# Kernel tuning notes

Hardware: AMD Instinct MI355X
Metric: run time of the kernel (lower is better)

Reference implementation:

```python
import jax, jax.numpy as jnp
import numpy as np

B, T, U, V = 8, 128, 64, 1024
BLANK = V - 1  # blank=-1 resolves to last class index


def setup_inputs() -> dict:
    key = jax.random.key(0)
    k1, k2, k3, k4 = jax.random.split(key, 4)
    logits = jax.random.normal(k1, (B, T, U + 1, V), dtype=jnp.float32)
    targets = jax.random.randint(k2, (B, U), 0, V - 1, dtype=jnp.int32)  # exclude blank
    logit_lengths = jax.random.randint(k3, (B,), T // 2, T + 1, dtype=jnp.int32)
    target_lengths = jax.random.randint(k4, (B,), U // 2, U + 1, dtype=jnp.int32)
    return {
        "logits": logits,
        "targets": targets,
        "logit_lengths": logit_lengths,
        "target_lengths": target_lengths,
    }


def _rnnt_neglogp(logits, targets, logit_lengths, target_lengths, blank):
    """RNNT forward-variable DP (Graves 2012). Returns per-sample -log p(y|x)."""
    Bn, Tn, U1, Vn = logits.shape
    Un = U1 - 1
    lp = jax.nn.log_softmax(logits, axis=-1)  # fused_log_softmax=True
    lp_blank = lp[..., blank]                                  # (B, T, U+1)
    idx = jnp.broadcast_to(targets[:, None, :, None], (Bn, Tn, Un, 1))
    lp_emit = jnp.take_along_axis(lp[:, :, :Un, :], idx, axis=-1)[..., 0]  # (B, T, U)

    # alpha[t, u]: log-prob of emitting first u labels using first t frames.
    # alpha[0, u] = sum_{v<u} emit(0, v)
    row0 = jnp.concatenate(
        [jnp.zeros((Bn, 1), lp.dtype), jnp.cumsum(lp_emit[:, 0, :], axis=-1)], axis=1
    )  # (B, U+1)

    def inner(a_prev, x):
        # a[u] = logaddexp(alpha[t-1,u] + blank(t-1,u),  a[u-1] + emit(t,u-1))
        b_u, e_u = x
        a_new = jnp.logaddexp(b_u, a_prev + e_u)
        return a_new, a_new

    def outer(prev_row, x):
        blank_prev, emit_t = x  # (B, U+1), (B, U)
        b_term = prev_row + blank_prev  # vertical (blank) transition term
        _, rest = jax.lax.scan(
            inner, b_term[:, 0], (b_term[:, 1:].T, emit_t.T)
        )  # rest: (U, B)
        new_row = jnp.concatenate([b_term[:, :1], rest.T], axis=1)  # (B, U+1)
        return new_row, new_row

    xs = (
        jnp.swapaxes(lp_blank[:, :-1, :], 0, 1),  # (T-1, B, U+1)
        jnp.swapaxes(lp_emit[:, 1:, :], 0, 1),    # (T-1, B, U)
    )
    _, rows = jax.lax.scan(outer, row0, xs)
    alpha = jnp.concatenate([row0[None], rows], axis=0)  # (T, B, U+1)

    bidx = jnp.arange(Bn)
    t_last = logit_lengths - 1
    u_last = target_lengths
    a_end = alpha[t_last, bidx, u_last]
    final_blank = lp_blank[bidx, t_last, u_last]
    return -(a_end + final_blank)


def reference(logits, targets, logit_lengths, target_lengths):
    return _rnnt_neglogp(logits, targets, logit_lengths, target_lengths, BLANK)
```

## Files before the change

### kernel.cpp

```cpp
#include <hip/hip_runtime.h>
#include <hip/hip_bf16.h>

#define BB 8
#define TT 128
#define UU 64
#define VV 1024
#define U1 65
#define NROWS (BB * TT * U1)
#define NDIAG (TT + UU)
#define DSZ (NDIAG * U1)
#define NPROD (NROWS / 4)
#define KPF 8

typedef unsigned long long ull;

__device__ __forceinline__ float wave_sum64(float v) {
#pragma unroll
    for (int off = 32; off; off >>= 1) v += __shfl_xor(v, off, 64);
    return v;
}

__device__ __forceinline__ float2 ldP(const ull* Pb, int idx) {
    union { ull u; float2 f; } c;
    c.u = __hip_atomic_load(Pb + idx, __ATOMIC_RELAXED, __HIP_MEMORY_SCOPE_AGENT);
    return c.f;
}

__device__ __forceinline__ int diag_need(int c) {
    return min(c, 64) - max(0, c - 127) + 1;
}

__device__ __forceinline__ void wait_diag(const unsigned int* cb, int c) {
    const int nd = diag_need(c);
    int guard = 0;
    while ((int)__hip_atomic_load(cb + c, __ATOMIC_RELAXED,
                                  __HIP_MEMORY_SCOPE_AGENT) < nd) {
        __builtin_amdgcn_s_sleep(1);
        if (++guard > (1 << 22)) break;
    }
}

__global__ __launch_bounds__(256) void rnnt_fused_kernel(
    const float* __restrict__ logits, const int* __restrict__ targets,
    const int* __restrict__ logit_lengths, const int* __restrict__ target_lengths,
    ull* __restrict__ P, unsigned int* __restrict__ cnt,
    float* __restrict__ out) {

    if (blockIdx.x >= BB) {
        const int wave = threadIdx.x >> 6;
        const int lane = threadIdx.x & 63;
        const int row  = (blockIdx.x - BB) * 4 + wave;
        const int b   = row / (TT * U1);
        const int rem = row - b * (TT * U1);
        const int t   = rem / U1;
        const int u   = rem - t * U1;

        const float4* p4 = (const float4*)(logits + (size_t)row * VV);
        float4 x0 = p4[lane];
        float4 x1 = p4[lane + 64];
        float4 x2 = p4[lane + 128];
        float4 x3 = p4[lane + 192];

        float s = __expf(x0.x) + __expf(x0.y) + __expf(x0.z) + __expf(x0.w)
                + __expf(x1.x) + __expf(x1.y) + __expf(x1.z) + __expf(x1.w)
                + __expf(x2.x) + __expf(x2.y) + __expf(x2.z) + __expf(x2.w)
                + __expf(x3.x) + __expf(x3.y) + __expf(x3.z) + __expf(x3.w);
        s = wave_sum64(s);
        const float lse = __logf(s);

        const float blankv = __shfl(x3.w, 63, 64) - lse;
        float emitv = 0.f;
        if (u < UU) {
            const int tgt = targets[b * UU + u];
            const int qq = tgt >> 2, grp = qq >> 6, sl = qq & 63, c4 = tgt & 3;
            float4 g4 = (grp == 0) ? x0 : (grp == 1) ? x1 : (grp == 2) ? x2 : x3;
            float cv = (c4 == 0) ? g4.x : (c4 == 1) ? g4.y : (c4 == 2) ? g4.z : g4.w;
            emitv = __shfl(cv, sl, 64) - lse;
        }
        if (lane == 0) {
            union { ull u; float2 f; } pk;
            pk.f = make_float2(blankv, emitv);
            const int d = t + u;
            __hip_atomic_store(P + (size_t)b * DSZ + d * U1 + u, pk.u,
                               __ATOMIC_RELAXED, __HIP_MEMORY_SCOPE_AGENT);
            asm volatile("s_waitcnt vmcnt(0)" ::: "memory");
            __hip_atomic_fetch_add(cnt + b * NDIAG + d, 1u,
                                   __ATOMIC_RELAXED, __HIP_MEMORY_SCOPE_AGENT);
        }
        return;
    }

    if (threadIdx.x >= 64) return;
    const int b = blockIdx.x;
    const int l = threadIdx.x;
    const ull* Pb = P + (size_t)b * DSZ;
    const unsigned int* cb = cnt + b * NDIAG;
    const int tl = logit_lengths[b] - 1;
    const int ul = target_lengths[b];
    const int Dfin = tl + ul;

    const float NEG = -1e30f;
    float aprev   = (l == 0) ? 0.f : NEG;
    float aprev64 = NEG;
    float res = 0.f;

    float2 ring[KPF], ring64[KPF];
#pragma unroll
    for (int k = 0; k < KPF; ++k) {
        wait_diag(cb, k);
        ring[k]   = ldP(Pb, k * U1 + l);
        ring64[k] = ldP(Pb, k * U1 + 64);
    }

    for (int base = 1; base <= NDIAG - 1; base += KPF) {
#pragma unroll
        for (int s = 0; s < KPF; ++s) {
            const int d = base + s;
            if (d > NDIAG - 1) break;
            float2 pr   = ring[s];
            float2 p64v = ring64[s];
            float edl = __shfl_up(pr.y, 1, 64);
            float al  = __shfl_up(aprev, 1, 64);
            const int t = d - l;
            float va = (t >= 1) ? aprev + pr.x : NEG;
            float vb = (l >= 1) ? al + edl : NEG;
            float mm = fmaxf(va, vb);
            float r  = mm + __logf(__expf(va - mm) + __expf(vb - mm));
            r = (t >= 0 && t < TT) ? r : NEG;
            const int t64 = d - 64;
            float va64 = (t64 >= 1) ? aprev64 + p64v.x : NEG;
            float vb64 = aprev + pr.y;
            float mm64 = fmaxf(va64, vb64);
            float r64  = mm64 + __logf(__expf(va64 - mm64) + __expf(vb64 - mm64));
            r64 = (t64 >= 0) ? r64 : NEG;
            if (d == Dfin) {
                if (ul < 64) { if (l == ul) res = r; }
                else if (l == 63) res = r64;
            }
            aprev = r; aprev64 = r64;
            const int c2 = d - 1 + KPF;
            if (c2 <= NDIAG - 2) {
                wait_diag(cb, c2);
                ring[s]   = ldP(Pb, c2 * U1 + l);
                ring64[s] = ldP(Pb, c2 * U1 + 64);
            }
        }
    }

    const float rr = __shfl(res, (ul < 64) ? ul : 63, 64);
    if (l == 0) {
        wait_diag(cb, Dfin);
        out[b] = -(rr + ldP(Pb, Dfin * U1 + ul).x);
    }
}

extern "C" void kernel_launch(void* const* d_in, const int* in_sizes, int n_in,
                              void* d_out, int out_size, void* d_ws, size_t ws_size,
                              hipStream_t stream) {
    const float* logits         = (const float*)d_in[0];
    const int*   targets        = (const int*)d_in[1];
    const int*   logit_lengths  = (const int*)d_in[2];
    const int*   target_lengths = (const int*)d_in[3];
    float* outp = (float*)d_out;

    ull* P = (ull*)d_ws;
    unsigned int* cnt = (unsigned int*)((char*)d_ws + (1 << 20));

    hipMemsetAsync(cnt, 0, BB * NDIAG * sizeof(unsigned int), stream);
    rnnt_fused_kernel<<<BB + NPROD, 256, 0, stream>>>(
        logits, targets, logit_lengths, target_lengths, P, cnt, outp);
}
```

Before: 470.3 us.

## Replace per-diagonal counters with sentinel-valued data polling for producer-consumer sync

```diff
diff --git a/kernel.cpp b/kernel.cpp
--- a/kernel.cpp
+++ b/kernel.cpp
@@ -13,6 +13,7 @@
 #define KPF 8
 
 typedef unsigned long long ull;
+#define SENT32 0xFFFFFFFFu
 
 __device__ __forceinline__ float wave_sum64(float v) {
 #pragma unroll
@@ -20,31 +21,20 @@
     return v;
 }
 
-__device__ __forceinline__ float2 ldP(const ull* Pb, int idx) {
-    union { ull u; float2 f; } c;
-    c.u = __hip_atomic_load(Pb + idx, __ATOMIC_RELAXED, __HIP_MEMORY_SCOPE_AGENT);
-    return c.f;
+__device__ __forceinline__ ull ldPu(const ull* Pb, int idx) {
+    return __hip_atomic_load(Pb + idx, __ATOMIC_RELAXED, __HIP_MEMORY_SCOPE_AGENT);
 }
-
-__device__ __forceinline__ int diag_need(int c) {
-    return min(c, 64) - max(0, c - 127) + 1;
+__device__ __forceinline__ bool nrdy(ull v) {
+    return ((unsigned)(v >> 32) == SENT32) | ((unsigned)v == SENT32);
 }
-
-__device__ __forceinline__ void wait_diag(const unsigned int* cb, int c) {
-    const int nd = diag_need(c);
-    int guard = 0;
-    while ((int)__hip_atomic_load(cb + c, __ATOMIC_RELAXED,
-                                  __HIP_MEMORY_SCOPE_AGENT) < nd) {
-        __builtin_amdgcn_s_sleep(1);
-        if (++guard > (1 << 22)) break;
-    }
+__device__ __forceinline__ float2 u2f(ull v) {
+    union { ull u; float2 f; } c; c.u = v; return c.f;
 }
 
 __global__ __launch_bounds__(256) void rnnt_fused_kernel(
     const float* __restrict__ logits, const int* __restrict__ targets,
     const int* __restrict__ logit_lengths, const int* __restrict__ target_lengths,
-    ull* __restrict__ P, unsigned int* __restrict__ cnt,
-    float* __restrict__ out) {
+    ull* __restrict__ P, float* __restrict__ out) {
 
     if (blockIdx.x >= BB) {
         const int wave = threadIdx.x >> 6;
@@ -80,12 +70,8 @@
         if (lane == 0) {
             union { ull u; float2 f; } pk;
             pk.f = make_float2(blankv, emitv);
-            const int d = t + u;
-            __hip_atomic_store(P + (size_t)b * DSZ + d * U1 + u, pk.u,
+            __hip_atomic_store(P + (size_t)b * DSZ + (t + u) * U1 + u, pk.u,
                                __ATOMIC_RELAXED, __HIP_MEMORY_SCOPE_AGENT);
-            asm volatile("s_waitcnt vmcnt(0)" ::: "memory");
-            __hip_atomic_fetch_add(cnt + b * NDIAG + d, 1u,
-                                   __ATOMIC_RELAXED, __HIP_MEMORY_SCOPE_AGENT);
         }
         return;
     }
@@ -94,7 +80,6 @@
     const int b = blockIdx.x;
     const int l = threadIdx.x;
     const ull* Pb = P + (size_t)b * DSZ;
-    const unsigned int* cb = cnt + b * NDIAG;
     const int tl = logit_lengths[b] - 1;
     const int ul = target_lengths[b];
     const int Dfin = tl + ul;
@@ -104,12 +89,11 @@
     float aprev64 = NEG;
     float res = 0.f;
 
-    float2 ring[KPF], ring64[KPF];
+    ull ring[KPF], ring64[KPF];
 #pragma unroll
     for (int k = 0; k < KPF; ++k) {
-        wait_diag(cb, k);
-        ring[k]   = ldP(Pb, k * U1 + l);
-        ring64[k] = ldP(Pb, k * U1 + 64);
+        ring[k]   = ldPu(Pb, k * U1 + l);
+        ring64[k] = ldPu(Pb, k * U1 + 64);
     }
 
     for (int base = 1; base <= NDIAG - 1; base += KPF) {
@@ -117,8 +101,18 @@
         for (int s = 0; s < KPF; ++s) {
             const int d = base + s;
             if (d > NDIAG - 1) break;
-            float2 pr   = ring[s];
-            float2 p64v = ring64[s];
+            const int c = d - 1;
+            ull pu = ring[s], qu = ring64[s];
+            const bool pex = (c >= l) && (c - l <= TT - 1);
+            const bool qex = (c >= 64);
+            int guard = 0;
+            while (__ballot((pex && nrdy(pu)) || (qex && nrdy(qu)))) {
+                pu = ldPu(Pb, c * U1 + l);
+                qu = ldPu(Pb, c * U1 + 64);
+                if (++guard > (1 << 18)) break;
+            }
+            float2 pr   = u2f(pu);
+            float2 p64v = u2f(qu);
             float edl = __shfl_up(pr.y, 1, 64);
             float al  = __shfl_up(aprev, 1, 64);
             const int t = d - l;
@@ -138,19 +132,20 @@
                 else if (l == 63) res = r64;
             }
             aprev = r; aprev64 = r64;
-            const int c2 = d - 1 + KPF;
+            const int c2 = c + KPF;
             if (c2 <= NDIAG - 2) {
-                wait_diag(cb, c2);
-                ring[s]   = ldP(Pb, c2 * U1 + l);
-                ring64[s] = ldP(Pb, c2 * U1 + 64);
+                ring[s]   = ldPu(Pb, c2 * U1 + l);
+                ring64[s] = ldPu(Pb, c2 * U1 + 64);
             }
         }
     }
 
     const float rr = __shfl(res, (ul < 64) ? ul : 63, 64);
     if (l == 0) {
-        wait_diag(cb, Dfin);
-        out[b] = -(rr + ldP(Pb, Dfin * U1 + ul).x);
+        ull v = ldPu(Pb, Dfin * U1 + ul);
+        int guard = 0;
+        while (nrdy(v) && ++guard < (1 << 18)) v = ldPu(Pb, Dfin * U1 + ul);
+        out[b] = -(rr + u2f(v).x);
     }
 }
 
@@ -164,9 +159,8 @@
     float* outp = (float*)d_out;
 
     ull* P = (ull*)d_ws;
-    unsigned int* cnt = (unsigned int*)((char*)d_ws + (1 << 20));
 
-    hipMemsetAsync(cnt, 0, BB * NDIAG * sizeof(unsigned int), stream);
+    hipMemsetAsync(P, 0xFF, (size_t)BB * DSZ * sizeof(ull), stream);
     rnnt_fused_kernel<<<BB + NPROD, 256, 0, stream>>>(
-        logits, targets, logit_lengths, target_lengths, P, cnt, outp);
+        logits, targets, logit_lengths, target_lengths, P, outp);
 }
```

Result: faster. 459.2 us (-2.3%).
